# Kernel optimization log

Measured on AMD Instinct MI355X. Metric: run time of the kernel, lower is better.

The kernel has to match this reference:

```python
import jax, jax.numpy as jnp
import numpy as np


def setup_inputs() -> dict:
    key = jax.random.key(0)
    k1, k2, k3, k4, k5 = jax.random.split(key, 5)
    B, Cin, D, H, W = 16, 16, 32, 32, 32
    Cout, Kd = 32, 3
    return {
        "x": jax.random.normal(k1, (B, Cin, D, H, W), dtype=jnp.float32),
        "weight": jax.random.normal(k2, (Cout, Cin, Kd, Kd, Kd), dtype=jnp.float32),
        "conv_bias": jax.random.normal(k3, (Cout,), dtype=jnp.float32),
        "scaling_factor": jax.random.normal(k4, (Cout, 1, 1, 1), dtype=jnp.float32),
        "bias_param": jax.random.normal(k5, (Cout, 1, 1, 1), dtype=jnp.float32),
    }


def reference(x, weight, conv_bias, scaling_factor, bias_param):
    # 3D valid conv, stride 1, NCDHW layout / OIDHW kernel
    y = jax.lax.conv_general_dilated(
        x, weight,
        window_strides=(1, 1, 1),
        padding="VALID",
        dimension_numbers=("NCDHW", "OIDHW", "NCDHW"),
    )
    # per-channel bias, scale, tanh, scale, sigmoid (broadcast over D,H,W)
    y = y + conv_bias[None, :, None, None, None]
    y = jnp.tanh(y * scaling_factor[None]) * bias_param[None]
    return jax.nn.sigmoid(y)
```

## Files before the change

### kernel.cpp

```cpp
#include <hip/hip_runtime.h>

#define NB    16
#define CIN   16
#define COUT  32
#define DIN   32
#define DOUT  30

typedef __attribute__((ext_vector_type(8)))  short        short8;
typedef __attribute__((ext_vector_type(4)))  unsigned int uint4v;
typedef __attribute__((ext_vector_type(16))) float        f32x16;

#define XWS_OFS_SHORTS   28672
#define XWS_PART_SHORTS  8388608
#define WS_NEED          (57344 + 2ull * 16 * 1024 * 1024)

static __device__ __forceinline__ unsigned short f2bf_rne(float f) {
    unsigned int u = __builtin_bit_cast(unsigned int, f);
    u += 0x7fffu + ((u >> 16) & 1u);
    return (unsigned short)(u >> 16);
}
static __device__ __forceinline__ float bf2f(unsigned short s) {
    unsigned int u = ((unsigned int)s) << 16;
    return __builtin_bit_cast(float, u);
}
static __device__ __forceinline__ unsigned int cvt_pk_bf16(float a, float b) {
    unsigned int r;
    asm("v_cvt_pk_bf16_f32 %0, %1, %2" : "=v"(r) : "v"(a), "v"(b));
    return r;
}
static __device__ __forceinline__ void gload_lds16(const short* g, short* l) {
    __builtin_amdgcn_global_load_lds(
        (const __attribute__((address_space(1))) void*)g,
        (__attribute__((address_space(3))) void*)l, 16, 0, 0);
}

__global__ __launch_bounds__(64) void repack_w(const float* __restrict__ wgt,
                                               short* __restrict__ ws) {
    const int s  = blockIdx.x;
    const int l  = threadIdx.x;
    const int co  = l & 31;
    const int ci0 = (l >> 5) * 8;
    short8 vh, vl;
#pragma unroll
    for (int j = 0; j < 8; ++j) {
        float f = wgt[co * (CIN * 27) + (ci0 + j) * 27 + s];
        unsigned short h = f2bf_rne(f);
        vh[j] = (short)h;
        vl[j] = (short)f2bf_rne(f - bf2f(h));
    }
    ((short8*)ws)[s * 64 + l]            = vh;
    ((short8*)ws)[27 * 64 + s * 64 + l]  = vl;
}

__global__ __launch_bounds__(256) void repack_x(const float* __restrict__ x,
                                                short* __restrict__ xws) {
    const int rp  = blockIdx.x * 4 + (threadIdx.x >> 6);
    const int l   = threadIdx.x & 63;
    const int hi8 = l >> 5, w = l & 31;
    const int b   = rp >> 10;
    const int dh  = rp & 1023;
    const int gbase = b * (CIN * 32768) + hi8 * 8 * 32768 + dh * 32 + w;
    float f[8];
#pragma unroll
    for (int j = 0; j < 8; ++j) f[j] = x[gbase + j * 32768];
    uint4v vh, vl;
#pragma unroll
    for (int j = 0; j < 8; j += 2) {
        unsigned int hp = cvt_pk_bf16(f[j], f[j + 1]);
        float b0 = __builtin_bit_cast(float, hp << 16);
        float b1 = __builtin_bit_cast(float, hp & 0xffff0000u);
        unsigned int lp = cvt_pk_bf16(f[j] - b0, f[j + 1] - b1);
        vh[j >> 1] = hp;
        vl[j >> 1] = lp;
    }
    ((uint4v*)xws)[rp * 64 + l]               = vh;
    ((uint4v*)xws)[1048576 + rp * 64 + l]     = vl;
}

__global__ __launch_bounds__(512, 6) void conv3d_mfma_v2(
    const short* __restrict__ xws,
    const short* __restrict__ wsA,
    const float* __restrict__ cbias,
    const float* __restrict__ scal,
    const float* __restrict__ bpar,
    float* __restrict__ out)
{
    __shared__ __align__(16) short sx[2 * 12288];
    __shared__ float sp[96];

    const int htile = blockIdx.x;
    const int dpair = blockIdx.y;
    const int b     = blockIdx.z;

    const int tid  = threadIdx.x;
    const int ww   = tid >> 6;
    const int wd   = ww >> 2;
    const int wy   = ww & 3;
    const int lane = tid & 63;

    if (tid < 32) {
        sp[tid]      = cbias[tid];
        sp[32 + tid] = scal[tid];
        sp[64 + tid] = bpar[tid];
    }

    const int h0 = htile * 4;
    const int d0 = dpair * 2;

#pragma unroll
    for (int t = 0; t < 3; ++t) {
        const int rpl = ww + t * 8;
        const int dz  = rpl / 6;
        const int row = rpl - dz * 6;
        int h_in = h0 + row; if (h_in > 31) h_in = 31;
        const int grp = (b * 32 + (d0 + dz)) * 32 + h_in;
        const short* g0 = xws + (size_t)grp * 512 + lane * 8;
        const short* g1 = xws + XWS_PART_SHORTS + (size_t)grp * 512 + lane * 8;
        gload_lds16(g0, sx + rpl * 512);
        gload_lds16(g1, sx + 12288 + rpl * 512);
    }
    __syncthreads();

    const int h = h0 + wy;
    if (h >= DOUT) return;
    const int d = d0 + wd;

    const int n  = lane & 31;
    const int hi = lane >> 5;

    int wofs[3];
#pragma unroll
    for (int kw = 0; kw < 3; ++kw) {
        int wc = n + kw; if (wc > 31) wc = 31;
        wofs[kw] = hi * 256 + wc * 8;
    }

    f32x16 acc0, acc1;
#pragma unroll
    for (int i = 0; i < 16; ++i) { acc0[i] = 0.0f; acc1[i] = 0.0f; }

    const short8* wa = (const short8*)wsA;
    short8 ah = wa[lane];
    short8 al = wa[1728 + lane];
#pragma unroll
    for (int s = 0; s < 27; ++s) {
        const int kd = s / 9, r9 = s - kd * 9, kh = r9 / 3, kw = r9 - kh * 3;
        const int rbase = ((wd + kd) * 6 + wy + kh) * 512;
        short8 bh = *(const short8*)(sx + rbase + wofs[kw]);
        short8 bl = *(const short8*)(sx + 12288 + rbase + wofs[kw]);
        const int sn = (s < 26) ? s + 1 : 26;
        short8 anh = wa[sn * 64 + lane];
        short8 anl = wa[1728 + sn * 64 + lane];
        if (s & 1) {
            acc1 = __builtin_amdgcn_mfma_f32_32x32x16_bf16(ah, bh, acc1, 0, 0, 0);
            acc1 = __builtin_amdgcn_mfma_f32_32x32x16_bf16(ah, bl, acc1, 0, 0, 0);
            acc1 = __builtin_amdgcn_mfma_f32_32x32x16_bf16(al, bh, acc1, 0, 0, 0);
        } else {
            acc0 = __builtin_amdgcn_mfma_f32_32x32x16_bf16(ah, bh, acc0, 0, 0, 0);
            acc0 = __builtin_amdgcn_mfma_f32_32x32x16_bf16(ah, bl, acc0, 0, 0, 0);
            acc0 = __builtin_amdgcn_mfma_f32_32x32x16_bf16(al, bh, acc0, 0, 0, 0);
        }
        ah = anh; al = anl;
    }
#pragma unroll
    for (int i = 0; i < 16; ++i) acc0[i] += acc1[i];

    if (n < DOUT) {
        const int obase = b * (COUT * DOUT * DOUT * DOUT)
                        + d * (DOUT * DOUT) + h * DOUT + n;
#pragma unroll
        for (int r = 0; r < 16; ++r) {
            const int co = (r & 3) + 8 * (r >> 2) + 4 * hi;
            float y  = acc0[r] + sp[co];
            float t  = y * sp[32 + co];
            float th = 1.0f - 2.0f / (__expf(2.0f * t) + 1.0f);
            float z  = th * sp[64 + co];
            float rr = 1.0f / (1.0f + __expf(-z));
            out[obase + co * (DOUT * DOUT * DOUT)] = rr;
        }
    }
}

__global__ __launch_bounds__(512) void conv3d_mfma_v1(
    const float* __restrict__ x,
    const short* __restrict__ wsA,
    const float* __restrict__ cbias,
    const float* __restrict__ scal,
    const float* __restrict__ bpar,
    float* __restrict__ out)
{
    __shared__ __align__(16) short sx[2 * 12288];
    __shared__ float sp[96];

    const int htile = blockIdx.x;
    const int dpair = blockIdx.y;
    const int b     = blockIdx.z;

    const int tid  = threadIdx.x;
    const int ww   = tid >> 6;
    const int wd   = ww >> 2;
    const int wy   = ww & 3;
    const int lane = tid & 63;

    if (tid < 32) {
        sp[tid]      = cbias[tid];
        sp[32 + tid] = scal[tid];
        sp[64 + tid] = bpar[tid];
    }

    const int h0 = htile * 4;
    const int d0 = dpair * 2;

    const int xb = b * (CIN * DIN * DIN * DIN);
    for (int c = tid; c < 1536; c += 512) {
        const int w   = c & 31;
        const int hi8 = (c >> 5) & 1;
        const int rr  = c >> 6;
        const int dz  = rr / 6;
        const int row = rr - dz * 6;
        int h_in = h0 + row; if (h_in > 31) h_in = 31;
        const int gbase = xb + (hi8 * 8) * (DIN * DIN * DIN)
                        + (d0 + dz) * (DIN * DIN) + h_in * DIN + w;
        float f[8];
#pragma unroll
        for (int j = 0; j < 8; ++j) f[j] = x[gbase + j * (DIN * DIN * DIN)];
        uint4v vh, vl;
#pragma unroll
        for (int j = 0; j < 8; j += 2) {
            unsigned int hp = cvt_pk_bf16(f[j], f[j + 1]);
            float b0 = __builtin_bit_cast(float, hp << 16);
            float b1 = __builtin_bit_cast(float, hp & 0xffff0000u);
            unsigned int lp = cvt_pk_bf16(f[j] - b0, f[j + 1] - b1);
            vh[j >> 1] = hp;
            vl[j >> 1] = lp;
        }
        const int idx = rr * 64 + hi8 * 32 + w;
        *(uint4v*)(sx + idx * 8)         = vh;
        *(uint4v*)(sx + 12288 + idx * 8) = vl;
    }
    __syncthreads();

    const int h = h0 + wy;
    if (h >= DOUT) return;
    const int d = d0 + wd;

    const int n  = lane & 31;
    const int hi = lane >> 5;

    int wofs[3];
#pragma unroll
    for (int kw = 0; kw < 3; ++kw) {
        int wc = n + kw; if (wc > 31) wc = 31;
        wofs[kw] = hi * 256 + wc * 8;
    }

    f32x16 acc;
#pragma unroll
    for (int i = 0; i < 16; ++i) acc[i] = 0.0f;

    const short8* wa = (const short8*)wsA;
#pragma unroll
    for (int kd = 0; kd < 3; ++kd) {
#pragma unroll
        for (int kh = 0; kh < 3; ++kh) {
            const int rbase = ((wd + kd) * 6 + wy + kh) * 512;
#pragma unroll
            for (int kw = 0; kw < 3; ++kw) {
                const int s = kd * 9 + kh * 3 + kw;
                short8 ah = wa[s * 64 + lane];
                short8 al = wa[1728 + s * 64 + lane];
                short8 bh = *(const short8*)(sx + rbase + wofs[kw]);
                short8 bl = *(const short8*)(sx + 12288 + rbase + wofs[kw]);
                acc = __builtin_amdgcn_mfma_f32_32x32x16_bf16(ah, bh, acc, 0, 0, 0);
                acc = __builtin_amdgcn_mfma_f32_32x32x16_bf16(ah, bl, acc, 0, 0, 0);
                acc = __builtin_amdgcn_mfma_f32_32x32x16_bf16(al, bh, acc, 0, 0, 0);
            }
        }
    }

    if (n < DOUT) {
        const int obase = b * (COUT * DOUT * DOUT * DOUT)
                        + d * (DOUT * DOUT) + h * DOUT + n;
#pragma unroll
        for (int r = 0; r < 16; ++r) {
            const int co = (r & 3) + 8 * (r >> 2) + 4 * hi;
            float y  = acc[r] + sp[co];
            float t  = y * sp[32 + co];
            float th = 1.0f - 2.0f / (__expf(2.0f * t) + 1.0f);
            float z  = th * sp[64 + co];
            float rr = 1.0f / (1.0f + __expf(-z));
            out[obase + co * (DOUT * DOUT * DOUT)] = rr;
        }
    }
}

extern "C" void kernel_launch(void* const* d_in, const int* in_sizes, int n_in,
                              void* d_out, int out_size, void* d_ws, size_t ws_size,
                              hipStream_t stream) {
    const float* x     = (const float*)d_in[0];
    const float* wgt   = (const float*)d_in[1];
    const float* cbias = (const float*)d_in[2];
    const float* scal  = (const float*)d_in[3];
    const float* bpar  = (const float*)d_in[4];
    float* out = (float*)d_out;
    short* ws  = (short*)d_ws;

    hipLaunchKernelGGL(repack_w, dim3(27), dim3(64), 0, stream, wgt, ws);

    if (ws_size >= WS_NEED) {
        short* xws = ws + XWS_OFS_SHORTS;
        hipLaunchKernelGGL(repack_x, dim3(4096), dim3(256), 0, stream, x, xws);
        hipLaunchKernelGGL(conv3d_mfma_v2, dim3(8, 15, NB), dim3(512), 0, stream,
                           xws, ws, cbias, scal, bpar, out);
    } else {
        hipLaunchKernelGGL(conv3d_mfma_v1, dim3(8, 15, NB), dim3(512), 0, stream,
                           x, ws, cbias, scal, bpar, out);
    }
}
```

Measured before the change: 157.9 us.

## Compute both output depth slices per wave to reuse weight and LDS loads

Each block drops from 8 waves to 4, and each wave now computes two adjacent output depth slices with two accumulators. Within each (kh,kw) step, one LDS input row is loaded once and feeds both slices, and the weight fragments for the three kd values are loaded once. This cuts redundant weight loads from global or cache and redundant LDS reads, at the cost of more registers per wave, fewer waves per block, and a fully unrolled, longer MFMA chain per wave.

```diff
diff --git a/kernel.cpp b/kernel.cpp
--- a/kernel.cpp
+++ b/kernel.cpp
@@ -77,7 +77,7 @@
     ((uint4v*)xws)[1048576 + rp * 64 + l]     = vl;
 }
 
-__global__ __launch_bounds__(512, 6) void conv3d_mfma_v2(
+__global__ __launch_bounds__(256, 3) void conv3d_mfma_v3(
     const short* __restrict__ xws,
     const short* __restrict__ wsA,
     const float* __restrict__ cbias,
@@ -94,8 +94,6 @@
 
     const int tid  = threadIdx.x;
     const int ww   = tid >> 6;
-    const int wd   = ww >> 2;
-    const int wy   = ww & 3;
     const int lane = tid & 63;
 
     if (tid < 32) {
@@ -108,8 +106,8 @@
     const int d0 = dpair * 2;
 
 #pragma unroll
-    for (int t = 0; t < 3; ++t) {
-        const int rpl = ww + t * 8;
+    for (int t = 0; t < 6; ++t) {
+        const int rpl = ww + t * 4;
         const int dz  = rpl / 6;
         const int row = rpl - dz * 6;
         int h_in = h0 + row; if (h_in > 31) h_in = 31;
@@ -121,18 +119,18 @@
     }
     __syncthreads();
 
-    const int h = h0 + wy;
+    const int wy = ww;
+    const int h  = h0 + wy;
     if (h >= DOUT) return;
-    const int d = d0 + wd;
 
     const int n  = lane & 31;
     const int hi = lane >> 5;
 
-    int wofs[3];
+    const short* pb[3];
 #pragma unroll
     for (int kw = 0; kw < 3; ++kw) {
         int wc = n + kw; if (wc > 31) wc = 31;
-        wofs[kw] = hi * 256 + wc * 8;
+        pb[kw] = sx + wy * 512 + hi * 256 + wc * 8;
     }
 
     f32x16 acc0, acc1;
@@ -140,43 +138,54 @@
     for (int i = 0; i < 16; ++i) { acc0[i] = 0.0f; acc1[i] = 0.0f; }
 
     const short8* wa = (const short8*)wsA;
-    short8 ah = wa[lane];
-    short8 al = wa[1728 + lane];
-#pragma unroll
-    for (int s = 0; s < 27; ++s) {
-        const int kd = s / 9, r9 = s - kd * 9, kh = r9 / 3, kw = r9 - kh * 3;
-        const int rbase = ((wd + kd) * 6 + wy + kh) * 512;
-        short8 bh = *(const short8*)(sx + rbase + wofs[kw]);
-        short8 bl = *(const short8*)(sx + 12288 + rbase + wofs[kw]);
-        const int sn = (s < 26) ? s + 1 : 26;
-        short8 anh = wa[sn * 64 + lane];
-        short8 anl = wa[1728 + sn * 64 + lane];
-        if (s & 1) {
-            acc1 = __builtin_amdgcn_mfma_f32_32x32x16_bf16(ah, bh, acc1, 0, 0, 0);
-            acc1 = __builtin_amdgcn_mfma_f32_32x32x16_bf16(ah, bl, acc1, 0, 0, 0);
-            acc1 = __builtin_amdgcn_mfma_f32_32x32x16_bf16(al, bh, acc1, 0, 0, 0);
-        } else {
-            acc0 = __builtin_amdgcn_mfma_f32_32x32x16_bf16(ah, bh, acc0, 0, 0, 0);
-            acc0 = __builtin_amdgcn_mfma_f32_32x32x16_bf16(ah, bl, acc0, 0, 0, 0);
-            acc0 = __builtin_amdgcn_mfma_f32_32x32x16_bf16(al, bh, acc0, 0, 0, 0);
-        }
-        ah = anh; al = anl;
-    }
-#pragma unroll
-    for (int i = 0; i < 16; ++i) acc0[i] += acc1[i];
+#pragma unroll
+    for (int e = 0; e < 9; ++e) {
+        const int kh = e / 3, kw = e - kh * 3;
+        short8 Ah[3], Al[3];
+#pragma unroll
+        for (int g = 0; g < 3; ++g) {
+            Ah[g] = wa[(g * 9 + e) * 64 + lane];
+            Al[g] = wa[1728 + (g * 9 + e) * 64 + lane];
+        }
+        const short* base = pb[kw] + kh * 512;
+#pragma unroll
+        for (int dz = 0; dz < 4; ++dz) {
+            short8 bh = *(const short8*)(base + dz * 3072);
+            short8 bl = *(const short8*)(base + 12288 + dz * 3072);
+            if (dz < 3) {
+                acc0 = __builtin_amdgcn_mfma_f32_32x32x16_bf16(Ah[dz], bh, acc0, 0, 0, 0);
+                acc0 = __builtin_amdgcn_mfma_f32_32x32x16_bf16(Ah[dz], bl, acc0, 0, 0, 0);
+                acc0 = __builtin_amdgcn_mfma_f32_32x32x16_bf16(Al[dz], bh, acc0, 0, 0, 0);
+            }
+            if (dz > 0) {
+                acc1 = __builtin_amdgcn_mfma_f32_32x32x16_bf16(Ah[dz - 1], bh, acc1, 0, 0, 0);
+                acc1 = __builtin_amdgcn_mfma_f32_32x32x16_bf16(Ah[dz - 1], bl, acc1, 0, 0, 0);
+                acc1 = __builtin_amdgcn_mfma_f32_32x32x16_bf16(Al[dz - 1], bh, acc1, 0, 0, 0);
+            }
+        }
+    }
 
     if (n < DOUT) {
         const int obase = b * (COUT * DOUT * DOUT * DOUT)
-                        + d * (DOUT * DOUT) + h * DOUT + n;
+                        + d0 * (DOUT * DOUT) + h * DOUT + n;
 #pragma unroll
         for (int r = 0; r < 16; ++r) {
             const int co = (r & 3) + 8 * (r >> 2) + 4 * hi;
-            float y  = acc0[r] + sp[co];
-            float t  = y * sp[32 + co];
-            float th = 1.0f - 2.0f / (__expf(2.0f * t) + 1.0f);
-            float z  = th * sp[64 + co];
-            float rr = 1.0f / (1.0f + __expf(-z));
-            out[obase + co * (DOUT * DOUT * DOUT)] = rr;
+            const float cb = sp[co], sc = sp[32 + co], bp = sp[64 + co];
+            {
+                float y  = acc0[r] + cb;
+                float t  = y * sc;
+                float th = 1.0f - 2.0f / (__expf(2.0f * t) + 1.0f);
+                float z  = th * bp;
+                out[obase + co * (DOUT * DOUT * DOUT)] = 1.0f / (1.0f + __expf(-z));
+            }
+            {
+                float y  = acc1[r] + cb;
+                float t  = y * sc;
+                float th = 1.0f - 2.0f / (__expf(2.0f * t) + 1.0f);
+                float z  = th * bp;
+                out[obase + (DOUT * DOUT) + co * (DOUT * DOUT * DOUT)] = 1.0f / (1.0f + __expf(-z));
+            }
         }
     }
 }
@@ -310,7 +319,7 @@
     if (ws_size >= WS_NEED) {
         short* xws = ws + XWS_OFS_SHORTS;
         hipLaunchKernelGGL(repack_x, dim3(4096), dim3(256), 0, stream, x, xws);
-        hipLaunchKernelGGL(conv3d_mfma_v2, dim3(8, 15, NB), dim3(512), 0, stream,
+        hipLaunchKernelGGL(conv3d_mfma_v3, dim3(8, 15, NB), dim3(256), 0, stream,
                            xws, ws, cbias, scal, bpar, out);
     } else {
         hipLaunchKernelGGL(conv3d_mfma_v1, dim3(8, 15, NB), dim3(512), 0, stream,
```

After: 150.5 us. 4.7% less time.
